# Kernel tuning notes

Measured on AMD Instinct MI355X. Metric: run time of the kernel, lower is better.

## Reference

```python
import jax, jax.numpy as jnp
import numpy as np

LN_EPS = 1e-5
B, T, D, H, NB, HH = 256, 128, 512, 1024, 64, 8


def _layernorm(x, g, b):
    m = x.mean(-1, keepdims=True)
    v = ((x - m) ** 2).mean(-1, keepdims=True)
    return (x - m) / jnp.sqrt(v + LN_EPS) * g + b


def setup_inputs() -> dict:
    key = jax.random.key(0)
    ks = jax.random.split(key, 10)
    init = lambda k, shape, fan: jax.random.normal(k, shape, jnp.float32) * np.float32(1.0 / np.sqrt(fan))
    return {
        "context_features": jax.random.normal(ks[0], (B, T, D), jnp.float32),
        "beam_history": jax.random.randint(ks[1], (B, HH), 0, NB),
        "beam_embed": init(ks[2], (NB, D), D),
        "W_in": init(ks[3], (H, 2 * D), 2 * D), "b_in": jnp.zeros((H,), jnp.float32),
        "W_init": init(ks[4], (H, 2 * D), 2 * D), "b_init": jnp.zeros((H,), jnp.float32),
        "W_ih": init(ks[5], (3 * H, H), H), "b_ih": jnp.zeros((3 * H,), jnp.float32),
        "W_hh": init(ks[6], (3 * H, H), H), "b_hh": jnp.zeros((3 * H,), jnp.float32),
        "ln_g": jnp.ones((H,), jnp.float32), "ln_b": jnp.zeros((H,), jnp.float32),
        "W_o1": init(ks[7], (H, H + D), H + D), "b_o1": jnp.zeros((H,), jnp.float32),
        "W_o2": init(ks[8], (NB, H), H), "b_o2": jnp.zeros((NB,), jnp.float32),
    }


def reference(context_features, beam_history, beam_embed, W_in, b_in, W_init, b_init,
              W_ih, b_ih, W_hh, b_hh, ln_g, ln_b, W_o1, b_o1, W_o2, b_o2):
    # --- init: history embedding mean + global context mean -> initial GRU state ---
    prev0 = beam_history[:, -1]                      # (B,)
    hist_emb = beam_embed[beam_history].mean(axis=1)  # (B, D)
    ctx_global = context_features.mean(axis=1)        # (B, D)
    h0 = jnp.tanh(jnp.concatenate([ctx_global, hist_emb], axis=-1) @ W_init.T + b_init)  # (B, H)

    def step(carry, ctx_t):
        h, prev = carry
        prev_emb = beam_embed[prev]                                            # (B, D)
        x = jax.nn.relu(jnp.concatenate([ctx_t, prev_emb], -1) @ W_in.T + b_in)  # (B, H)
        # PyTorch GRUCell: gate order r, z, n
        gx = x @ W_ih.T + b_ih
        gh = h @ W_hh.T + b_hh
        xr, xz, xn = jnp.split(gx, 3, axis=-1)
        hr, hz, hn = jnp.split(gh, 3, axis=-1)
        r = jax.nn.sigmoid(xr + hr)
        z = jax.nn.sigmoid(xz + hz)
        n = jnp.tanh(xn + r * hn)
        h_new = (1.0 - z) * n + z * h
        h_norm = _layernorm(h_new, ln_g, ln_b)
        o = jax.nn.relu(jnp.concatenate([h_norm, ctx_t], -1) @ W_o1.T + b_o1)
        logits_t = o @ W_o2.T + b_o2                                            # (B, NB)
        pred_next = jnp.argmax(logits_t, axis=-1)
        return (h_new, pred_next), logits_t

    ctx_tbd = jnp.swapaxes(context_features, 0, 1)  # (T, B, D)
    (_, _), logits = jax.lax.scan(step, (h0, prev0), ctx_tbd)
    return jnp.swapaxes(logits, 0, 1)  # (B, T, NB) == ar_logits
```

## Files before the change

kernel.cpp:

```cpp
#include <hip/hip_runtime.h>
#include <hip/hip_bf16.h>


#define TS 68
#define LDPA 40
constexpr int SZ = 262144;
constexpr int TT = 128;
constexpr int LDA_CTX = 65536;

typedef __attribute__((ext_vector_type(8))) short short8_t;
typedef __attribute__((ext_vector_type(4))) float f32x4;


__device__ __forceinline__ unsigned short f2bf_rne(float v) {
    unsigned u = __float_as_uint(v);
    unsigned r = u + 0x7fffu + ((u >> 16) & 1u);
    return (unsigned short)(r >> 16);
}
__device__ __forceinline__ float bfbits2f(unsigned short h) {
    return __uint_as_float(((unsigned)h) << 16);
}
__device__ __forceinline__ void split2(float v, unsigned short& h, unsigned short& l) {
    h = f2bf_rne(v);
    l = f2bf_rne(v - bfbits2f(h));
}


__device__ __forceinline__ void mfma_core7(
    const unsigned short* __restrict__ Ah, const unsigned short* __restrict__ Al,
    int lda, int b0,
    const unsigned short* __restrict__ Bh, const unsigned short* __restrict__ Bl,
    int ldb, int n0, int k0base, int nIter,
    unsigned short* sm, f32x4 acc[2][4])
{
    const int tid = threadIdx.x, lane = tid & 63, wid = tid >> 6;
    const int wr = wid >> 1, wc = wid & 1;
    const int l15 = lane & 15, kg = (lane >> 4) * 8;
    const int arow = tid >> 2, acol = (tid & 3) * 8;
    const int brow = tid >> 1, bcol = (tid & 1) * 16;

    const int AOFF = 2560, BHOFF = 5120, BLOFF = 10240, BUF = 15360;

    const unsigned short* gAh = Ah + (size_t)(b0 + arow) * lda + k0base + acol;
    const unsigned short* gAl = Al + (size_t)(b0 + arow) * lda + k0base + acol;
    const unsigned short* gBh = Bh + (size_t)(n0 + brow) * ldb + k0base + bcol;
    const unsigned short* gBl = Bl + (size_t)(n0 + brow) * ldb + k0base + bcol;

    {
        short8_t a_h = *(const short8_t*)gAh;
        short8_t a_l = *(const short8_t*)gAl;
        short8_t bh0 = *(const short8_t*)gBh;
        short8_t bh1 = *(const short8_t*)(gBh + 8);
        short8_t bl0 = *(const short8_t*)gBl;
        short8_t bl1 = *(const short8_t*)(gBl + 8);
        *(short8_t*)&sm[arow * LDPA + acol]              = a_h;
        *(short8_t*)&sm[AOFF + arow * LDPA + acol]       = a_l;
        *(short8_t*)&sm[BHOFF + brow * LDPA + bcol]      = bh0;
        *(short8_t*)&sm[BHOFF + brow * LDPA + bcol + 8]  = bh1;
        *(short8_t*)&sm[BLOFF + brow * LDPA + bcol]      = bl0;
        *(short8_t*)&sm[BLOFF + brow * LDPA + bcol + 8]  = bl1;
    }
    __syncthreads();

    int cur = 0;
    const int aro = (wr * 32 + l15) * LDPA + kg;
    for (int i = 0; i < nIter; ++i) {
        short8_t a_h, a_l, bh0, bh1, bl0, bl1;
        if (i + 1 < nIter) {
            const int ko = (i + 1) * 32;
            a_h = *(const short8_t*)(gAh + ko);
            a_l = *(const short8_t*)(gAl + ko);
            bh0 = *(const short8_t*)(gBh + ko);
            bh1 = *(const short8_t*)(gBh + ko + 8);
            bl0 = *(const short8_t*)(gBl + ko);
            bl1 = *(const short8_t*)(gBl + ko + 8);
        }
        const unsigned short* S = sm + cur * BUF;
        short8_t afh[2], afl[2];
#pragma unroll
        for (int mi = 0; mi < 2; ++mi) {
            afh[mi] = *(const short8_t*)&S[aro + mi * 16 * LDPA];
            afl[mi] = *(const short8_t*)&S[AOFF + aro + mi * 16 * LDPA];
        }
#pragma unroll
        for (int ni = 0; ni < 4; ++ni) {
            const int bro = (wc * 64 + ni * 16 + l15) * LDPA + kg;
            short8_t b_h = *(const short8_t*)&S[BHOFF + bro];
            short8_t b_l = *(const short8_t*)&S[BLOFF + bro];
#pragma unroll
            for (int mi = 0; mi < 2; ++mi) {
                acc[mi][ni] = __builtin_amdgcn_mfma_f32_16x16x32_bf16(afh[mi], b_h, acc[mi][ni], 0, 0, 0);
                acc[mi][ni] = __builtin_amdgcn_mfma_f32_16x16x32_bf16(afh[mi], b_l, acc[mi][ni], 0, 0, 0);
                acc[mi][ni] = __builtin_amdgcn_mfma_f32_16x16x32_bf16(afl[mi], b_h, acc[mi][ni], 0, 0, 0);
            }
        }
        if (i + 1 < nIter) {
            unsigned short* N_ = sm + (cur ^ 1) * BUF;
            *(short8_t*)&N_[arow * LDPA + acol]             = a_h;
            *(short8_t*)&N_[AOFF + arow * LDPA + acol]      = a_l;
            *(short8_t*)&N_[BHOFF + brow * LDPA + bcol]     = bh0;
            *(short8_t*)&N_[BHOFF + brow * LDPA + bcol + 8] = bh1;
            *(short8_t*)&N_[BLOFF + brow * LDPA + bcol]     = bl0;
            *(short8_t*)&N_[BLOFF + brow * LDPA + bcol + 8] = bl1;
        }
        __syncthreads();
        cur ^= 1;
    }
}


__device__ __forceinline__ void gemm_tile64(
    const float* __restrict__ A, int lda, int Mlim, int b0,
    const float* __restrict__ W, int ldw, int n0, int K,
    float* At, float* Wt, float acc[4][4])
{
    const int tid = threadIdx.x;
    const int tx = tid & 15, ty = tid >> 4;
    const int r = tid >> 2, c0 = (tid & 3) << 2;
    for (int k0 = 0; k0 < K; k0 += 16) {
        float4 av = make_float4(0.f, 0.f, 0.f, 0.f);
        if (b0 + r < Mlim)
            av = *(const float4*)(A + (size_t)(b0 + r) * lda + k0 + c0);
        float4 wv = *(const float4*)(W + (size_t)(n0 + r) * ldw + k0 + c0);
        __syncthreads();
        At[(c0+0)*TS + r] = av.x; At[(c0+1)*TS + r] = av.y;
        At[(c0+2)*TS + r] = av.z; At[(c0+3)*TS + r] = av.w;
        Wt[(c0+0)*TS + r] = wv.x; Wt[(c0+1)*TS + r] = wv.y;
        Wt[(c0+2)*TS + r] = wv.z; Wt[(c0+3)*TS + r] = wv.w;
        __syncthreads();
#pragma unroll
        for (int kk = 0; kk < 16; ++kk) {
            float4 a = *(const float4*)(At + kk*TS + ty*4);
            float4 w = *(const float4*)(Wt + kk*TS + tx*4);
            acc[0][0] += a.x*w.x; acc[0][1] += a.x*w.y; acc[0][2] += a.x*w.z; acc[0][3] += a.x*w.w;
            acc[1][0] += a.y*w.x; acc[1][1] += a.y*w.y; acc[1][2] += a.y*w.z; acc[1][3] += a.y*w.w;
            acc[2][0] += a.z*w.x; acc[2][1] += a.z*w.y; acc[2][2] += a.z*w.z; acc[2][3] += a.z*w.w;
            acc[3][0] += a.w*w.x; acc[3][1] += a.w*w.y; acc[3][2] += a.w*w.z; acc[3][3] += a.w*w.w;
        }
    }
}


__global__ void pre0_kernel(const float* __restrict__ ctx, const int* __restrict__ bh,
                            const float* __restrict__ be, float* __restrict__ A0,
                            int* __restrict__ prev)
{
    int b = blockIdx.x, tid = threadIdx.x;
    float s = 0.f;
    for (int t = 0; t < TT; ++t) s += ctx[(size_t)b * LDA_CTX + t * 512 + tid];
    A0[b * 1024 + tid] = s * (1.f / 128.f);
    float s2 = 0.f;
    for (int i = 0; i < 8; ++i) s2 += be[bh[b * 8 + i] * 512 + tid];
    A0[b * 1024 + 512 + tid] = s2 * 0.125f;
    if (tid == 0) prev[b] = bh[b * 8 + 7];
}

__global__ void copy_gb_kernel(const float* g, const float* bb, float* gb)
{
    int idx = blockIdx.x * 256 + threadIdx.x;
    if (idx < 1024) gb[idx] = g[idx];
    else            gb[idx] = bb[idx - 1024];
}

__global__ void wo2t_kernel(const float* __restrict__ W_o2, float* __restrict__ Wo2t)
{
    int idx = blockIdx.x * 256 + threadIdx.x;
    int k = idx >> 6, n = idx & 63;
    Wo2t[idx] = W_o2[n * 1024 + k];
}

__global__ void wsplit_kernel(const float* __restrict__ src, int src_ld, int col0,
                              int N, int K, const float* __restrict__ scale,
                              unsigned short* __restrict__ hi,
                              unsigned short* __restrict__ lo)
{
    int idx = blockIdx.x * 256 + threadIdx.x;
    if (idx >= N * K) return;
    int n = idx / K, k = idx - n * K;
    float v = src[(size_t)n * src_ld + col0 + k];
    if (scale) v *= scale[k];
    unsigned short h, l;
    split2(v, h, l);
    hi[idx] = h; lo[idx] = l;
}

__global__ void gemm64_kernel(const float* __restrict__ A, int lda, int M,
                              const float* __restrict__ W, int ldw, int K,
                              const float* __restrict__ bias,
                              float* __restrict__ C, int ldc, int act)
{
    __shared__ __align__(16) float At[16 * TS];
    __shared__ __align__(16) float Wt[16 * TS];
    float acc[4][4] = {};
    int b0 = blockIdx.x * 64, n0 = blockIdx.y * 64;
    gemm_tile64(A, lda, M, b0, W, ldw, n0, K, At, Wt, acc);
    int tx = threadIdx.x & 15, ty = threadIdx.x >> 4;
#pragma unroll
    for (int i = 0; i < 4; ++i) {
        int b = b0 + ty * 4 + i;
        if (b >= M) continue;
#pragma unroll
        for (int j = 0; j < 4; ++j) {
            int n = n0 + tx * 4 + j;
            float v = acc[i][j] + (bias ? bias[n] : 0.f);
            if (act == 1) v = tanhf(v);
            C[(size_t)b * ldc + n] = v;
        }
    }
}

__global__ void xbuild0s_kernel(const float* __restrict__ cin0, const float* __restrict__ bpart,
                                const int* __restrict__ prev,
                                unsigned short* __restrict__ xh, unsigned short* __restrict__ xl)
{
    int b = blockIdx.x, tid = threadIdx.x;
    int pb = prev[b];
#pragma unroll
    for (int jj = 0; jj < 4; ++jj) {
        int j = jj * 256 + tid;
        float v = fmaxf(cin0[(size_t)b * 1024 + j] + bpart[(size_t)pb * 1024 + j], 0.f);
        unsigned short h, l;
        split2(v, h, l);
        xh[(size_t)b * 1024 + j] = h;
        xl[(size_t)b * 1024 + j] = l;
    }
}

__global__ void xbuild0_kernel(const float* __restrict__ cin0, const float* __restrict__ bpart,
                               const int* __restrict__ prev, float* __restrict__ x)
{
    int b = blockIdx.x, tid = threadIdx.x;
    int pb = prev[b];
#pragma unroll
    for (int jj = 0; jj < 4; ++jj) {
        int j = jj * 256 + tid;
        x[(size_t)b * 1024 + j] = fmaxf(cin0[(size_t)b * 1024 + j] + bpart[(size_t)pb * 1024 + j], 0.f);
    }
}


__global__ __launch_bounds__(256) void gates7_kernel(
    const unsigned short* __restrict__ xh, const unsigned short* __restrict__ xl,
    const unsigned short* __restrict__ hh, const unsigned short* __restrict__ hl,
    const unsigned short* __restrict__ ctxh, const unsigned short* __restrict__ ctxl,
    const unsigned short* __restrict__ wih_hi, const unsigned short* __restrict__ wih_lo,
    const unsigned short* __restrict__ whh_hi, const unsigned short* __restrict__ whh_lo,
    const unsigned short* __restrict__ wcin_hi, const unsigned short* __restrict__ wcin_lo,
    const unsigned short* __restrict__ wo1c_hi, const unsigned short* __restrict__ wo1c_lo,
    const float* __restrict__ b_in, const float* __restrict__ b_o1,
    float* __restrict__ g6, float* __restrict__ cin, float* __restrict__ octx,
    int t)
{
    const int bid = blockIdx.x;
    const int z = bid & 7;
    const int tile = bid >> 3;
    const int tm = tile & 3, tn = tile >> 2;
    if (z == 6 && t + 1 >= TT) return;
    const int b0 = tm * 64, n0 = tn * 128;

    const unsigned short *Ah, *Al, *Bh, *Bl;
    int lda, ldb, nIter;
    const float* bias = nullptr;
    float* C;
    if (z < 6) {
        int g = z % 3, s = z / 3;
        Ah = s ? hh : xh; Al = s ? hl : xl; lda = 1024;
        Bh = (s ? whh_hi : wih_hi) + (size_t)g * 1048576;
        Bl = (s ? whh_lo : wih_lo) + (size_t)g * 1048576;
        ldb = 1024; nIter = 32;
        C = g6 + (size_t)z * SZ;
    } else if (z == 6) {
        int s = (t + 1) & 1;
        Ah = ctxh + (size_t)s * 131072; Al = ctxl + (size_t)s * 131072;
        lda = 512; ldb = 512; nIter = 16;
        Bh = wcin_hi; Bl = wcin_lo; bias = b_in; C = cin;
    } else {
        int s = t & 1;
        Ah = ctxh + (size_t)s * 131072; Al = ctxl + (size_t)s * 131072;
        lda = 512; ldb = 512; nIter = 16;
        Bh = wo1c_hi; Bl = wo1c_lo; bias = b_o1; C = octx;
    }

    __shared__ __align__(16) unsigned short sm[2 * 15360];
    f32x4 acc[2][4] = {};
    mfma_core7(Ah, Al, lda, b0, Bh, Bl, ldb, n0, 0, nIter, sm, acc);

    const int lane = threadIdx.x & 63, wid = threadIdx.x >> 6;
    const int wr = wid >> 1, wc = wid & 1;
    const int l15 = lane & 15, g4 = (lane >> 4) * 4;
#pragma unroll
    for (int mi = 0; mi < 2; ++mi) {
#pragma unroll
        for (int ni = 0; ni < 4; ++ni) {
            int col = n0 + wc * 64 + ni * 16 + l15;
            float bv = bias ? bias[col] : 0.f;
#pragma unroll
            for (int r = 0; r < 4; ++r) {
                int row = b0 + wr * 32 + mi * 16 + g4 + r;
                C[(size_t)row * 1024 + col] = acc[mi][ni][r] + bv;
            }
        }
    }
}

__global__ __launch_bounds__(256) void kb7_kernel(
    const unsigned short* __restrict__ hh, const unsigned short* __restrict__ hl,
    const unsigned short* __restrict__ wo1k_hi, const unsigned short* __restrict__ wo1k_lo,
    float* __restrict__ g6)
{
    const int bid = blockIdx.x;
    const int tm = bid >> 5, tn = (bid >> 2) & 7, p = bid & 3;
    const int b0 = tm * 64, n0 = tn * 128, k0 = p * 256;

    __shared__ __align__(16) unsigned short sm[2 * 15360];
    f32x4 acc[2][4] = {};
    mfma_core7(hh, hl, 1024, b0, wo1k_hi, wo1k_lo, 1024, n0, k0, 8, sm, acc);

    float* C = g6 + (size_t)p * SZ;
    const int lane = threadIdx.x & 63, wid = threadIdx.x >> 6;
    const int wr = wid >> 1, wc = wid & 1;
    const int l15 = lane & 15, g4 = (lane >> 4) * 4;
#pragma unroll
    for (int mi = 0; mi < 2; ++mi) {
#pragma unroll
        for (int ni = 0; ni < 4; ++ni) {
            int col = n0 + wc * 64 + ni * 16 + l15;
#pragma unroll
            for (int r = 0; r < 4; ++r) {
                int row = b0 + wr * 32 + mi * 16 + g4 + r;
                C[(size_t)row * 1024 + col] = acc[mi][ni][r];
            }
        }
    }
}

__global__ void gru_ln6_kernel(const float* __restrict__ g6,
                               const float* __restrict__ b_ih, const float* __restrict__ b_hh,
                               float* __restrict__ h,
                               unsigned short* __restrict__ hh, unsigned short* __restrict__ hl,
                               float* __restrict__ mbuf, float* __restrict__ isbuf)
{
    __shared__ float ls[4], lq[4];
    int b = blockIdx.x, tid = threadIdx.x;
    float s = 0.f, q = 0.f;
#pragma unroll
    for (int jj = 0; jj < 4; ++jj) {
        int j = jj * 256 + tid;
        size_t base = (size_t)b * 1024 + j;
        float xr = g6[0 * (size_t)SZ + base] + b_ih[j];
        float xz = g6[1 * (size_t)SZ + base] + b_ih[1024 + j];
        float xn = g6[2 * (size_t)SZ + base] + b_ih[2048 + j];
        float hr = g6[3 * (size_t)SZ + base] + b_hh[j];
        float hz = g6[4 * (size_t)SZ + base] + b_hh[1024 + j];
        float hn = g6[5 * (size_t)SZ + base] + b_hh[2048 + j];
        float r = 1.f / (1.f + expf(-(xr + hr)));
        float z = 1.f / (1.f + expf(-(xz + hz)));
        float nn = tanhf(xn + r * hn);
        float ho = h[base];
        float hv = (1.f - z) * nn + z * ho;
        h[base] = hv;
        unsigned short a, c;
        split2(hv, a, c); hh[base] = a; hl[base] = c;
        s += hv; q += hv * hv;
    }
    for (int off = 32; off; off >>= 1) {
        s += __shfl_down(s, off);
        q += __shfl_down(q, off);
    }
    int lane = tid & 63, w = tid >> 6;
    if (lane == 0) { ls[w] = s; lq[w] = q; }
    __syncthreads();
    if (tid == 0) {
        float S = ls[0] + ls[1] + ls[2] + ls[3];
        float Q = lq[0] + lq[1] + lq[2] + lq[3];
        float m = S * (1.f / 1024.f);
        mbuf[b] = m;
        isbuf[b] = rsqrtf(Q * (1.f / 1024.f) - m * m + 1e-5f);
    }
}

__global__ void kc7_kernel(const float* __restrict__ g6,
                           const float* __restrict__ Wo2t, const float* __restrict__ b_o2,
                           const float* __restrict__ uv, const float* __restrict__ octx,
                           const float* __restrict__ mbuf, const float* __restrict__ isbuf,
                           const float* __restrict__ cin, const float* __restrict__ bpart,
                           const float* __restrict__ ctx,
                           unsigned short* __restrict__ xh, unsigned short* __restrict__ xl,
                           unsigned short* __restrict__ ctxh, unsigned short* __restrict__ ctxl,
                           int* __restrict__ prev, float* __restrict__ out, int t)
{
    __shared__ __align__(16) float os[4][1024];
    __shared__ float red[4][4][64];
    __shared__ int sidx[4];
    const int b0 = blockIdx.x * 4, tid = threadIdx.x;

#pragma unroll
    for (int i = 0; i < 4; ++i) {
        int f = tid + i * 256;
        int r = f >> 8, c4 = (f & 255) << 2;
        size_t base = (size_t)(b0 + r) * 1024 + c4;
        float4 p0 = *(const float4*)(g6 + base);
        float4 p1 = *(const float4*)(g6 + (size_t)SZ + base);
        float4 p2 = *(const float4*)(g6 + 2 * (size_t)SZ + base);
        float4 p3 = *(const float4*)(g6 + 3 * (size_t)SZ + base);
        float4 oc = *(const float4*)(octx + base);
        float4 u4 = *(const float4*)(uv + c4);
        float4 v4 = *(const float4*)(uv + 1024 + c4);
        float m = mbuf[b0 + r], is = isbuf[b0 + r];
        float4 o4;
        o4.x = fmaxf((p0.x + p1.x + p2.x + p3.x - m * u4.x) * is + v4.x + oc.x, 0.f);
        o4.y = fmaxf((p0.y + p1.y + p2.y + p3.y - m * u4.y) * is + v4.y + oc.y, 0.f);
        o4.z = fmaxf((p0.z + p1.z + p2.z + p3.z - m * u4.z) * is + v4.z + oc.z, 0.f);
        o4.w = fmaxf((p0.w + p1.w + p2.w + p3.w - m * u4.w) * is + v4.w + oc.w, 0.f);
        *(float4*)&os[r][c4] = o4;
    }
    __syncthreads();

    {
        int n = tid & 63, seg = tid >> 6;
        float p0 = 0.f, p1 = 0.f, p2 = 0.f, p3 = 0.f;
        int k0 = seg * 256;
        for (int k = k0; k < k0 + 256; ++k) {
            float w = Wo2t[(size_t)k * 64 + n];
            p0 += os[0][k] * w; p1 += os[1][k] * w;
            p2 += os[2][k] * w; p3 += os[3][k] * w;
        }
        red[0][seg][n] = p0; red[1][seg][n] = p1;
        red[2][seg][n] = p2; red[3][seg][n] = p3;
    }
    __syncthreads();

    {
        int r = tid >> 6, n = tid & 63;
        float lg = red[r][0][n] + red[r][1][n] + red[r][2][n] + red[r][3][n] + b_o2[n];
        out[(size_t)(b0 + r) * (TT * 64) + t * 64 + n] = lg;
        float v = lg; int idx = n;
        for (int off = 32; off; off >>= 1) {
            float ov = __shfl_xor(v, off);
            int oi = __shfl_xor(idx, off);
            if (ov > v || (ov == v && oi < idx)) { v = ov; idx = oi; }
        }
        if (n == 0) { prev[b0 + r] = idx; sidx[r] = idx; }
    }
    __syncthreads();

    if (t + 1 < TT) {
#pragma unroll
        for (int i = 0; i < 16; ++i) {
            int idx = tid + i * 256;
            int r = idx >> 10, j = idx & 1023;
            float v = fmaxf(cin[(size_t)(b0 + r) * 1024 + j] +
                            bpart[(size_t)sidx[r] * 1024 + j], 0.f);
            unsigned short h, l;
            split2(v, h, l);
            xh[(size_t)(b0 + r) * 1024 + j] = h;
            xl[(size_t)(b0 + r) * 1024 + j] = l;
        }
    }
    if (t + 2 < TT) {
        int slot = t & 1;
#pragma unroll
        for (int i = 0; i < 8; ++i) {
            int idx = tid + i * 256;
            int r = idx >> 9, j = idx & 511;
            float v = ctx[(size_t)(b0 + r) * LDA_CTX + (t + 2) * 512 + j];
            unsigned short h, l;
            split2(v, h, l);
            ctxh[(size_t)slot * 131072 + (size_t)(b0 + r) * 512 + j] = h;
            ctxl[(size_t)slot * 131072 + (size_t)(b0 + r) * 512 + j] = l;
        }
    }
}


__global__ void step_gemms_kernel(
    const float* __restrict__ x, const float* __restrict__ hBase,
    const float* __restrict__ ctx,
    const float* __restrict__ Wih, const float* __restrict__ Whh,
    const float* __restrict__ Win, const float* __restrict__ Wo1,
    const float* __restrict__ b_in, const float* __restrict__ b_o1,
    float* __restrict__ g6, float* __restrict__ cinBase, float* __restrict__ octx,
    int t)
{
    __shared__ __align__(16) float At[16 * TS];
    __shared__ __align__(16) float Wt[16 * TS];
    float acc[4][4] = {};
    const int z = blockIdx.z, b0 = blockIdx.x * 64, n0 = blockIdx.y * 64;
    const float *A, *W, *bias = nullptr;
    float* C;
    int lda, ldw, K;
    if (z < 6) {
        int g = z % 3, s = z / 3;
        A = s ? (hBase + (size_t)(t & 1) * SZ) : x;
        lda = 1024;
        W = (s ? Whh : Wih) + (size_t)(g * 1024) * 1024;
        ldw = 1024; K = 1024;
        C = g6 + (size_t)z * SZ;
    } else if (z == 6) {
        if (t + 1 >= TT) return;
        A = ctx + (size_t)(t + 1) * 512; lda = LDA_CTX;
        W = Win; ldw = 1024; K = 512; bias = b_in;
        C = cinBase + (size_t)((t + 1) & 1) * SZ;
    } else {
        A = ctx + (size_t)t * 512; lda = LDA_CTX;
        W = Wo1 + 1024; ldw = 1536; K = 512; bias = b_o1;
        C = octx;
    }
    gemm_tile64(A, lda, 256, b0, W, ldw, n0, K, At, Wt, acc);
    int tx = threadIdx.x & 15, ty = threadIdx.x >> 4;
#pragma unroll
    for (int i = 0; i < 4; ++i) {
        int b = b0 + ty * 4 + i;
#pragma unroll
        for (int j = 0; j < 4; ++j) {
            int n = n0 + tx * 4 + j;
            float v = acc[i][j];
            if (bias) v += bias[n];
            C[(size_t)b * 1024 + n] = v;
        }
    }
}

__global__ void kb_kernel(const float* __restrict__ hg, const float* __restrict__ Wo1,
                          const float* __restrict__ uv, const float* __restrict__ octx,
                          const float* __restrict__ mbuf, const float* __restrict__ isbuf,
                          float* __restrict__ o)
{
    __shared__ __align__(16) float At[16 * TS];
    __shared__ __align__(16) float Wt[16 * TS];
    float acc[2][4] = {};
    const int b0 = blockIdx.x * 32, n0 = blockIdx.y * 64;
    const int tid = threadIdx.x, tx = tid & 15, ty = tid >> 4;
    const int r = tid >> 2, c0 = (tid & 3) << 2;
    for (int k0 = 0; k0 < 1024; k0 += 16) {
        float4 av = make_float4(0.f, 0.f, 0.f, 0.f);
        if (r < 32) av = *(const float4*)(hg + (size_t)(b0 + r) * 1024 + k0 + c0);
        float4 wv = *(const float4*)(Wo1 + (size_t)(n0 + r) * 1536 + k0 + c0);
        __syncthreads();
        At[(c0+0)*TS + r] = av.x; At[(c0+1)*TS + r] = av.y;
        At[(c0+2)*TS + r] = av.z; At[(c0+3)*TS + r] = av.w;
        Wt[(c0+0)*TS + r] = wv.x; Wt[(c0+1)*TS + r] = wv.y;
        Wt[(c0+2)*TS + r] = wv.z; Wt[(c0+3)*TS + r] = wv.w;
        __syncthreads();
#pragma unroll
        for (int kk = 0; kk < 16; ++kk) {
            float2 a = *(const float2*)(At + kk*TS + ty*2);
            float4 w = *(const float4*)(Wt + kk*TS + tx*4);
            acc[0][0] += a.x*w.x; acc[0][1] += a.x*w.y; acc[0][2] += a.x*w.z; acc[0][3] += a.x*w.w;
            acc[1][0] += a.y*w.x; acc[1][1] += a.y*w.y; acc[1][2] += a.y*w.z; acc[1][3] += a.y*w.w;
        }
    }
#pragma unroll
    for (int i = 0; i < 2; ++i) {
        int b = b0 + ty * 2 + i;
        float m = mbuf[b], is = isbuf[b];
#pragma unroll
        for (int j = 0; j < 4; ++j) {
            int n = n0 + tx * 4 + j;
            float v = (acc[i][j] - m * uv[n]) * is + uv[1024 + n] + octx[(size_t)b * 1024 + n];
            o[(size_t)b * 1024 + n] = fmaxf(v, 0.f);
        }
    }
}

__global__ void gru_ln_kernel(const float* __restrict__ g6,
                              const float* __restrict__ b_ih, const float* __restrict__ b_hh,
                              float* __restrict__ hBase, const float* __restrict__ ln_g,
                              float* __restrict__ hg, float* __restrict__ mbuf,
                              float* __restrict__ isbuf, int t)
{
    __shared__ float rs[256], rq[256];
    int b = blockIdx.x, tid = threadIdx.x;
    const float* hc = hBase + (size_t)(t & 1) * SZ + (size_t)b * 1024;
    float* hnx = hBase + (size_t)((t + 1) & 1) * SZ + (size_t)b * 1024;
    float s = 0.f, q = 0.f;
#pragma unroll
    for (int jj = 0; jj < 4; ++jj) {
        int j = jj * 256 + tid;
        size_t base = (size_t)b * 1024 + j;
        float xr = g6[0 * (size_t)SZ + base] + b_ih[j];
        float xz = g6[1 * (size_t)SZ + base] + b_ih[1024 + j];
        float xn = g6[2 * (size_t)SZ + base] + b_ih[2048 + j];
        float hr = g6[3 * (size_t)SZ + base] + b_hh[j];
        float hz = g6[4 * (size_t)SZ + base] + b_hh[1024 + j];
        float hn = g6[5 * (size_t)SZ + base] + b_hh[2048 + j];
        float r = 1.f / (1.f + expf(-(xr + hr)));
        float z = 1.f / (1.f + expf(-(xz + hz)));
        float nn = tanhf(xn + r * hn);
        float ho = hc[j];
        float hv = (1.f - z) * nn + z * ho;
        hnx[j] = hv;
        hg[base] = hv * ln_g[j];
        s += hv; q += hv * hv;
    }
    rs[tid] = s; rq[tid] = q;
    __syncthreads();
    for (int st = 128; st; st >>= 1) {
        if (tid < st) { rs[tid] += rs[tid + st]; rq[tid] += rq[tid + st]; }
        __syncthreads();
    }
    if (tid == 0) {
        float m = rs[0] * (1.f / 1024.f);
        float var = rq[0] * (1.f / 1024.f) - m * m;
        mbuf[b] = m;
        isbuf[b] = rsqrtf(var + 1e-5f);
    }
}

__global__ void kc_kernel(const float* __restrict__ o, const float* __restrict__ Wo2t,
                          const float* __restrict__ b_o2, const float* __restrict__ cinBase,
                          const float* __restrict__ bpart, float* __restrict__ x,
                          int* __restrict__ prev, float* __restrict__ out, int t)
{
    __shared__ __align__(16) float os[1024];
    __shared__ float red[4][64];
    __shared__ int sidx;
    int b = blockIdx.x, tid = threadIdx.x;
    const float* orow = o + (size_t)b * 1024;
    *(float4*)&os[tid * 4] = *(const float4*)&orow[tid * 4];
    __syncthreads();
    int n = tid & 63, seg = tid >> 6;
    float p = 0.f;
    int k0 = seg * 256;
#pragma unroll 8
    for (int k = 0; k < 256; ++k) p += os[k0 + k] * Wo2t[(size_t)(k0 + k) * 64 + n];
    red[seg][n] = p;
    __syncthreads();
    if (tid < 64) {
        float lg = red[0][tid] + red[1][tid] + red[2][tid] + red[3][tid] + b_o2[tid];
        out[((size_t)b * TT + t) * 64 + tid] = lg;
        float v = lg; int idx = tid;
        for (int off = 32; off; off >>= 1) {
            float ov = __shfl_xor(v, off);
            int oi = __shfl_xor(idx, off);
            if (ov > v || (ov == v && oi < idx)) { v = ov; idx = oi; }
        }
        if (tid == 0) { prev[b] = idx; sidx = idx; }
    }
    __syncthreads();
    if (t + 1 < TT) {
        int pb = sidx;
        const float* cn = cinBase + (size_t)((t + 1) & 1) * SZ + (size_t)b * 1024;
        const float* bp = bpart + (size_t)pb * 1024;
#pragma unroll
        for (int jj = 0; jj < 4; ++jj) {
            int j = jj * 256 + tid;
            x[(size_t)b * 1024 + j] = fmaxf(cn[j] + bp[j], 0.f);
        }
    }
}


extern "C" void kernel_launch(void* const* d_in, const int* in_sizes, int n_in,
                              void* d_out, int out_size, void* d_ws, size_t ws_size,
                              hipStream_t stream)
{
    const float* ctx    = (const float*)d_in[0];
    const int*   bh     = (const int*)d_in[1];
    const float* be     = (const float*)d_in[2];
    const float* W_in   = (const float*)d_in[3];
    const float* b_in   = (const float*)d_in[4];
    const float* W_init = (const float*)d_in[5];
    const float* b_init = (const float*)d_in[6];
    const float* W_ih   = (const float*)d_in[7];
    const float* b_ih   = (const float*)d_in[8];
    const float* W_hh   = (const float*)d_in[9];
    const float* b_hh   = (const float*)d_in[10];
    const float* ln_g   = (const float*)d_in[11];
    const float* ln_b   = (const float*)d_in[12];
    const float* W_o1   = (const float*)d_in[13];
    const float* b_o1   = (const float*)d_in[14];
    const float* W_o2   = (const float*)d_in[15];
    const float* b_o2   = (const float*)d_in[16];
    float* out = (float*)d_out;
    float* ws  = (float*)d_ws;

    const bool mfma_path = (ws_size >= 49830000ull);

    if (mfma_path) {
        float* hbuf  = ws;
        float* cin   = ws + 262144;
        float* octx  = ws + 524288;
        float* g6    = ws + 786432;
        float* A0    = g6;
        float* bpart = ws + 2359296;
        float* uvv   = ws + 2424832;
        float* gb    = ws + 2426880;
        float* Wo2t  = ws + 2428928;
        float* mbuf  = ws + 2494464;
        float* isbuf = ws + 2494720;
        int*   prev  = (int*)(ws + 2494976);
        unsigned short* bf = (unsigned short*)(ws + 2495232);
        unsigned short* wih_hi  = bf;
        unsigned short* wih_lo  = bf + 3145728;
        unsigned short* whh_hi  = bf + 6291456;
        unsigned short* whh_lo  = bf + 9437184;
        unsigned short* wo1k_hi = bf + 12582912;
        unsigned short* wo1k_lo = bf + 13631488;
        unsigned short* wo1c_hi = bf + 14680064;
        unsigned short* wo1c_lo = bf + 15204352;
        unsigned short* wcin_hi = bf + 15728640;
        unsigned short* wcin_lo = bf + 16252928;
        unsigned short* xh   = bf + 16777216;
        unsigned short* xl   = bf + 17039360;
        unsigned short* hh   = bf + 17301504;
        unsigned short* hl   = bf + 17563648;
        unsigned short* ctxh = bf + 17825792;
        unsigned short* ctxl = bf + 18087936;

        pre0_kernel<<<256, 512, 0, stream>>>(ctx, bh, be, A0, prev);
        copy_gb_kernel<<<8, 256, 0, stream>>>(ln_g, ln_b, gb);
        wo2t_kernel<<<256, 256, 0, stream>>>(W_o2, Wo2t);
        gemm64_kernel<<<dim3(4, 16), 256, 0, stream>>>(A0, 1024, 256, W_init, 1024, 1024,
                                                       b_init, hbuf, 1024, 1);
        gemm64_kernel<<<dim3(1, 16), 256, 0, stream>>>(be, 512, 64, W_in + 512, 1024, 512,
                                                       nullptr, bpart, 1024, 0);
        gemm64_kernel<<<dim3(1, 16), 256, 0, stream>>>(gb, 1024, 2, W_o1, 1536, 1024,
                                                       nullptr, uvv, 1024, 0);
        gemm64_kernel<<<dim3(4, 16), 256, 0, stream>>>(ctx, LDA_CTX, 256, W_in, 1024, 512,
                                                       b_in, cin, 1024, 0);
        xbuild0s_kernel<<<256, 256, 0, stream>>>(cin, bpart, prev, xh, xl);
        wsplit_kernel<<<12288, 256, 0, stream>>>(W_ih, 1024, 0, 3072, 1024, nullptr, wih_hi, wih_lo);
        wsplit_kernel<<<12288, 256, 0, stream>>>(W_hh, 1024, 0, 3072, 1024, nullptr, whh_hi, whh_lo);
        wsplit_kernel<<<4096, 256, 0, stream>>>(W_o1, 1536, 0, 1024, 1024, ln_g, wo1k_hi, wo1k_lo);
        wsplit_kernel<<<2048, 256, 0, stream>>>(W_o1, 1536, 1024, 1024, 512, nullptr, wo1c_hi, wo1c_lo);
        wsplit_kernel<<<2048, 256, 0, stream>>>(W_in, 1024, 0, 1024, 512, nullptr, wcin_hi, wcin_lo);
        wsplit_kernel<<<1024, 256, 0, stream>>>(hbuf, 1024, 0, 256, 1024, nullptr, hh, hl);
        wsplit_kernel<<<512, 256, 0, stream>>>(ctx, LDA_CTX, 0, 256, 512, nullptr, ctxh, ctxl);
        wsplit_kernel<<<512, 256, 0, stream>>>(ctx, LDA_CTX, 512, 256, 512, nullptr,
                                               ctxh + 131072, ctxl + 131072);

        for (int t = 0; t < TT; ++t) {
            gates7_kernel<<<256, 256, 0, stream>>>(
                xh, xl, hh, hl, ctxh, ctxl,
                wih_hi, wih_lo, whh_hi, whh_lo, wcin_hi, wcin_lo, wo1c_hi, wo1c_lo,
                b_in, b_o1, g6, cin, octx, t);
            gru_ln6_kernel<<<256, 256, 0, stream>>>(g6, b_ih, b_hh, hbuf,
                                                    hh, hl, mbuf, isbuf);
            kb7_kernel<<<128, 256, 0, stream>>>(hh, hl, wo1k_hi, wo1k_lo, g6);
            kc7_kernel<<<64, 256, 0, stream>>>(g6, Wo2t, b_o2, uvv, octx, mbuf, isbuf,
                                               cin, bpart, ctx, xh, xl, ctxh, ctxl,
                                               prev, out, t);
        }
    } else {
        float* A0    = ws;
        float* hbuf  = ws + 262144;
        float* hg    = ws + 786432;
        float* x     = ws + 1048576;
        float* cin   = ws + 1310720;
        float* octx  = ws + 1835008;
        float* g6    = ws + 2097152;
        float* obuf  = ws + 3670016;
        float* bpart = ws + 3932160;
        float* uvv   = ws + 3997696;
        float* gb    = ws + 3999744;
        float* Wo2t  = ws + 4001792;
        float* mbuf  = ws + 4067328;
        float* isbuf = ws + 4067584;
        int*   prev  = (int*)(ws + 4067840);

        pre0_kernel<<<256, 512, 0, stream>>>(ctx, bh, be, A0, prev);
        copy_gb_kernel<<<8, 256, 0, stream>>>(ln_g, ln_b, gb);
        wo2t_kernel<<<256, 256, 0, stream>>>(W_o2, Wo2t);
        gemm64_kernel<<<dim3(4, 16), 256, 0, stream>>>(A0, 1024, 256, W_init, 1024, 1024,
                                                       b_init, hbuf, 1024, 1);
        gemm64_kernel<<<dim3(1, 16), 256, 0, stream>>>(be, 512, 64, W_in + 512, 1024, 512,
                                                       nullptr, bpart, 1024, 0);
        gemm64_kernel<<<dim3(1, 16), 256, 0, stream>>>(gb, 1024, 2, W_o1, 1536, 1024,
                                                       nullptr, uvv, 1024, 0);
        gemm64_kernel<<<dim3(4, 16), 256, 0, stream>>>(ctx, LDA_CTX, 256, W_in, 1024, 512,
                                                       b_in, cin, 1024, 0);
        xbuild0_kernel<<<256, 256, 0, stream>>>(cin, bpart, prev, x);

        for (int t = 0; t < TT; ++t) {
            step_gemms_kernel<<<dim3(4, 16, 8), 256, 0, stream>>>(
                x, hbuf, ctx, W_ih, W_hh, W_in, W_o1, b_in, b_o1, g6, cin, octx, t);
            gru_ln_kernel<<<256, 256, 0, stream>>>(g6, b_ih, b_hh, hbuf, ln_g, hg,
                                                   mbuf, isbuf, t);
            kb_kernel<<<dim3(8, 16), 256, 0, stream>>>(hg, W_o1, uvv, octx, mbuf, isbuf, obuf);
            kc_kernel<<<256, 256, 0, stream>>>(obuf, Wo2t, b_o2, cin, bpart, x, prev, out, t);
        }
    }
}
```

Before: 7.913 ms.

## Fuse GRU+LayerNorm stats into output GEMM kernel and split fp32 activations on the fly

The separate GRU/LayerNorm kernel is folded into the kb kernel. Each block recomputes the GRU update for its 64x256 slice, writes h to a double-buffered fp32 array, and emits partial LN sums that kc combines. Activations (x, h, ctx) are now read as fp32 in the MFMA core and split into bf16 hi/lo while being staged into shared memory. This removes the pre-split hi/lo buffers, the ctx prefetch split, and one launch per timestep. In exchange, each block does extra split arithmetic in the inner loop, and the GRU elementwise work is repeated across the 8 column-tile blocks that share rows.

```diff
diff --git a/kernel.cpp b/kernel.cpp
--- a/kernel.cpp
+++ b/kernel.cpp
@@ -24,11 +24,22 @@
     h = f2bf_rne(v);
     l = f2bf_rne(v - bfbits2f(h));
 }
-
-
-__device__ __forceinline__ void mfma_core7(
-    const unsigned short* __restrict__ Ah, const unsigned short* __restrict__ Al,
-    int lda, int b0,
+__device__ __forceinline__ void splitA8(const float4& v0, const float4& v1,
+                                        short8_t& hi, short8_t& lo) {
+    unsigned short h[8], l[8];
+    split2(v0.x, h[0], l[0]); split2(v0.y, h[1], l[1]);
+    split2(v0.z, h[2], l[2]); split2(v0.w, h[3], l[3]);
+    split2(v1.x, h[4], l[4]); split2(v1.y, h[5], l[5]);
+    split2(v1.z, h[6], l[6]); split2(v1.w, h[7], l[7]);
+    hi = short8_t{(short)h[0],(short)h[1],(short)h[2],(short)h[3],
+                  (short)h[4],(short)h[5],(short)h[6],(short)h[7]};
+    lo = short8_t{(short)l[0],(short)l[1],(short)l[2],(short)l[3],
+                  (short)l[4],(short)l[5],(short)l[6],(short)l[7]};
+}
+
+
+__device__ __forceinline__ void mfma_core9(
+    const float* __restrict__ A, int lda, int b0,
     const unsigned short* __restrict__ Bh, const unsigned short* __restrict__ Bl,
     int ldb, int n0, int k0base, int nIter,
     unsigned short* sm, f32x4 acc[2][4])
@@ -41,20 +52,21 @@
 
     const int AOFF = 2560, BHOFF = 5120, BLOFF = 10240, BUF = 15360;
 
-    const unsigned short* gAh = Ah + (size_t)(b0 + arow) * lda + k0base + acol;
-    const unsigned short* gAl = Al + (size_t)(b0 + arow) * lda + k0base + acol;
+    const float* gA = A + (size_t)(b0 + arow) * lda + k0base + acol;
     const unsigned short* gBh = Bh + (size_t)(n0 + brow) * ldb + k0base + bcol;
     const unsigned short* gBl = Bl + (size_t)(n0 + brow) * ldb + k0base + bcol;
 
     {
-        short8_t a_h = *(const short8_t*)gAh;
-        short8_t a_l = *(const short8_t*)gAl;
+        float4 a0 = *(const float4*)gA;
+        float4 a1 = *(const float4*)(gA + 4);
+        short8_t ah, al;
+        splitA8(a0, a1, ah, al);
         short8_t bh0 = *(const short8_t*)gBh;
         short8_t bh1 = *(const short8_t*)(gBh + 8);
         short8_t bl0 = *(const short8_t*)gBl;
         short8_t bl1 = *(const short8_t*)(gBl + 8);
-        *(short8_t*)&sm[arow * LDPA + acol]              = a_h;
-        *(short8_t*)&sm[AOFF + arow * LDPA + acol]       = a_l;
+        *(short8_t*)&sm[arow * LDPA + acol]              = ah;
+        *(short8_t*)&sm[AOFF + arow * LDPA + acol]       = al;
         *(short8_t*)&sm[BHOFF + brow * LDPA + bcol]      = bh0;
         *(short8_t*)&sm[BHOFF + brow * LDPA + bcol + 8]  = bh1;
         *(short8_t*)&sm[BLOFF + brow * LDPA + bcol]      = bl0;
@@ -65,11 +77,12 @@
     int cur = 0;
     const int aro = (wr * 32 + l15) * LDPA + kg;
     for (int i = 0; i < nIter; ++i) {
-        short8_t a_h, a_l, bh0, bh1, bl0, bl1;
+        float4 a0, a1;
+        short8_t bh0, bh1, bl0, bl1;
         if (i + 1 < nIter) {
             const int ko = (i + 1) * 32;
-            a_h = *(const short8_t*)(gAh + ko);
-            a_l = *(const short8_t*)(gAl + ko);
+            a0 = *(const float4*)(gA + ko);
+            a1 = *(const float4*)(gA + ko + 4);
             bh0 = *(const short8_t*)(gBh + ko);
             bh1 = *(const short8_t*)(gBh + ko + 8);
             bl0 = *(const short8_t*)(gBl + ko);
@@ -95,9 +108,11 @@
             }
         }
         if (i + 1 < nIter) {
+            short8_t ah, al;
+            splitA8(a0, a1, ah, al);
             unsigned short* N_ = sm + (cur ^ 1) * BUF;
-            *(short8_t*)&N_[arow * LDPA + acol]             = a_h;
-            *(short8_t*)&N_[AOFF + arow * LDPA + acol]      = a_l;
+            *(short8_t*)&N_[arow * LDPA + acol]             = ah;
+            *(short8_t*)&N_[AOFF + arow * LDPA + acol]      = al;
             *(short8_t*)&N_[BHOFF + brow * LDPA + bcol]     = bh0;
             *(short8_t*)&N_[BHOFF + brow * LDPA + bcol + 8] = bh1;
             *(short8_t*)&N_[BLOFF + brow * LDPA + bcol]     = bl0;
@@ -155,18 +170,22 @@
     if (tid == 0) prev[b] = bh[b * 8 + 7];
 }
 
-__global__ void copy_gb_kernel(const float* g, const float* bb, float* gb)
-{
-    int idx = blockIdx.x * 256 + threadIdx.x;
-    if (idx < 1024) gb[idx] = g[idx];
-    else            gb[idx] = bb[idx - 1024];
-}
-
 __global__ void wo2t_kernel(const float* __restrict__ W_o2, float* __restrict__ Wo2t)
 {
     int idx = blockIdx.x * 256 + threadIdx.x;
     int k = idx >> 6, n = idx & 63;
     Wo2t[idx] = W_o2[n * 1024 + k];
+}
+
+__global__ void uv_kernel(const float* __restrict__ ln_g, const float* __restrict__ ln_b,
+                          const float* __restrict__ W_o1, float* __restrict__ uvv)
+{
+    int idx = blockIdx.x * 256 + threadIdx.x;
+    int which = idx >> 10, j = idx & 1023;
+    const float* vec = which ? ln_b : ln_g;
+    float s = 0.f;
+    for (int k = 0; k < 1024; ++k) s += vec[k] * W_o1[(size_t)j * 1536 + k];
+    uvv[which * 1024 + j] = s;
 }
 
 __global__ void wsplit_kernel(const float* __restrict__ src, int src_ld, int col0,
@@ -209,23 +228,6 @@
     }
 }
 
-__global__ void xbuild0s_kernel(const float* __restrict__ cin0, const float* __restrict__ bpart,
-                                const int* __restrict__ prev,
-                                unsigned short* __restrict__ xh, unsigned short* __restrict__ xl)
-{
-    int b = blockIdx.x, tid = threadIdx.x;
-    int pb = prev[b];
-#pragma unroll
-    for (int jj = 0; jj < 4; ++jj) {
-        int j = jj * 256 + tid;
-        float v = fmaxf(cin0[(size_t)b * 1024 + j] + bpart[(size_t)pb * 1024 + j], 0.f);
-        unsigned short h, l;
-        split2(v, h, l);
-        xh[(size_t)b * 1024 + j] = h;
-        xl[(size_t)b * 1024 + j] = l;
-    }
-}
-
 __global__ void xbuild0_kernel(const float* __restrict__ cin0, const float* __restrict__ bpart,
                                const int* __restrict__ prev, float* __restrict__ x)
 {
@@ -239,10 +241,9 @@
 }
 
 
-__global__ __launch_bounds__(256) void gates7_kernel(
-    const unsigned short* __restrict__ xh, const unsigned short* __restrict__ xl,
-    const unsigned short* __restrict__ hh, const unsigned short* __restrict__ hl,
-    const unsigned short* __restrict__ ctxh, const unsigned short* __restrict__ ctxl,
+__global__ __launch_bounds__(256) void gates9_kernel(
+    const float* __restrict__ xf, const float* __restrict__ hcur,
+    const float* __restrict__ ctx,
     const unsigned short* __restrict__ wih_hi, const unsigned short* __restrict__ wih_lo,
     const unsigned short* __restrict__ whh_hi, const unsigned short* __restrict__ whh_lo,
     const unsigned short* __restrict__ wcin_hi, const unsigned short* __restrict__ wcin_lo,
@@ -258,32 +259,31 @@
     if (z == 6 && t + 1 >= TT) return;
     const int b0 = tm * 64, n0 = tn * 128;
 
-    const unsigned short *Ah, *Al, *Bh, *Bl;
+    const float* A;
+    const unsigned short *Bh, *Bl;
     int lda, ldb, nIter;
     const float* bias = nullptr;
     float* C;
     if (z < 6) {
         int g = z % 3, s = z / 3;
-        Ah = s ? hh : xh; Al = s ? hl : xl; lda = 1024;
+        A = s ? hcur : xf; lda = 1024;
         Bh = (s ? whh_hi : wih_hi) + (size_t)g * 1048576;
         Bl = (s ? whh_lo : wih_lo) + (size_t)g * 1048576;
         ldb = 1024; nIter = 32;
         C = g6 + (size_t)z * SZ;
     } else if (z == 6) {
-        int s = (t + 1) & 1;
-        Ah = ctxh + (size_t)s * 131072; Al = ctxl + (size_t)s * 131072;
-        lda = 512; ldb = 512; nIter = 16;
+        A = ctx + (size_t)(t + 1) * 512; lda = LDA_CTX;
+        ldb = 512; nIter = 16;
         Bh = wcin_hi; Bl = wcin_lo; bias = b_in; C = cin;
     } else {
-        int s = t & 1;
-        Ah = ctxh + (size_t)s * 131072; Al = ctxl + (size_t)s * 131072;
-        lda = 512; ldb = 512; nIter = 16;
+        A = ctx + (size_t)t * 512; lda = LDA_CTX;
+        ldb = 512; nIter = 16;
         Bh = wo1c_hi; Bl = wo1c_lo; bias = b_o1; C = octx;
     }
 
     __shared__ __align__(16) unsigned short sm[2 * 15360];
     f32x4 acc[2][4] = {};
-    mfma_core7(Ah, Al, lda, b0, Bh, Bl, ldb, n0, 0, nIter, sm, acc);
+    mfma_core9(A, lda, b0, Bh, Bl, ldb, n0, 0, nIter, sm, acc);
 
     const int lane = threadIdx.x & 63, wid = threadIdx.x >> 6;
     const int wr = wid >> 1, wc = wid & 1;
@@ -303,21 +303,83 @@
     }
 }
 
-__global__ __launch_bounds__(256) void kb7_kernel(
-    const unsigned short* __restrict__ hh, const unsigned short* __restrict__ hl,
+__global__ __launch_bounds__(256) void kb9_kernel(
+    const float* __restrict__ g6,
+    const float* __restrict__ b_ih, const float* __restrict__ b_hh,
+    const float* __restrict__ hOld, float* __restrict__ hNew,
     const unsigned short* __restrict__ wo1k_hi, const unsigned short* __restrict__ wo1k_lo,
-    float* __restrict__ g6)
+    float* __restrict__ part, float* __restrict__ spq)
 {
     const int bid = blockIdx.x;
-    const int tm = bid >> 5, tn = (bid >> 2) & 7, p = bid & 3;
+    const int g = bid & 15, tn = bid >> 4;
+    const int tm = g >> 2, p = g & 3;
     const int b0 = tm * 64, n0 = tn * 128, k0 = p * 256;
+    const int tid = threadIdx.x;
+
+    {
+        const int r = tid >> 2, q = tid & 3;
+        const int row = b0 + r;
+        float s = 0.f, qs = 0.f;
+        for (int j = 0; j < 16; ++j) {
+            int c = k0 + j * 16 + q * 4;
+            size_t base = (size_t)row * 1024 + c;
+            float4 xr = *(const float4*)(g6 + base);
+            float4 xz = *(const float4*)(g6 + (size_t)SZ + base);
+            float4 xn = *(const float4*)(g6 + 2 * (size_t)SZ + base);
+            float4 hr = *(const float4*)(g6 + 3 * (size_t)SZ + base);
+            float4 hz = *(const float4*)(g6 + 4 * (size_t)SZ + base);
+            float4 hn = *(const float4*)(g6 + 5 * (size_t)SZ + base);
+            float4 ho = *(const float4*)(hOld + base);
+            float4 bi0 = *(const float4*)(b_ih + c);
+            float4 bi1 = *(const float4*)(b_ih + 1024 + c);
+            float4 bi2 = *(const float4*)(b_ih + 2048 + c);
+            float4 bh0 = *(const float4*)(b_hh + c);
+            float4 bh1 = *(const float4*)(b_hh + 1024 + c);
+            float4 bh2 = *(const float4*)(b_hh + 2048 + c);
+            float4 hv;
+            {
+                float rr = 1.f / (1.f + expf(-((xr.x + bi0.x) + (hr.x + bh0.x))));
+                float zz = 1.f / (1.f + expf(-((xz.x + bi1.x) + (hz.x + bh1.x))));
+                float nn = tanhf((xn.x + bi2.x) + rr * (hn.x + bh2.x));
+                hv.x = (1.f - zz) * nn + zz * ho.x;
+            }
+            {
+                float rr = 1.f / (1.f + expf(-((xr.y + bi0.y) + (hr.y + bh0.y))));
+                float zz = 1.f / (1.f + expf(-((xz.y + bi1.y) + (hz.y + bh1.y))));
+                float nn = tanhf((xn.y + bi2.y) + rr * (hn.y + bh2.y));
+                hv.y = (1.f - zz) * nn + zz * ho.y;
+            }
+            {
+                float rr = 1.f / (1.f + expf(-((xr.z + bi0.z) + (hr.z + bh0.z))));
+                float zz = 1.f / (1.f + expf(-((xz.z + bi1.z) + (hz.z + bh1.z))));
+                float nn = tanhf((xn.z + bi2.z) + rr * (hn.z + bh2.z));
+                hv.z = (1.f - zz) * nn + zz * ho.z;
+            }
+            {
+                float rr = 1.f / (1.f + expf(-((xr.w + bi0.w) + (hr.w + bh0.w))));
+                float zz = 1.f / (1.f + expf(-((xz.w + bi1.w) + (hz.w + bh1.w))));
+                float nn = tanhf((xn.w + bi2.w) + rr * (hn.w + bh2.w));
+                hv.w = (1.f - zz) * nn + zz * ho.w;
+            }
+            *(float4*)(hNew + base) = hv;
+            s += hv.x + hv.y + hv.z + hv.w;
+            qs += hv.x * hv.x + hv.y * hv.y + hv.z * hv.z + hv.w * hv.w;
+        }
+        s  += __shfl_xor(s, 1);  s  += __shfl_xor(s, 2);
+        qs += __shfl_xor(qs, 1); qs += __shfl_xor(qs, 2);
+        if (q == 0) {
+            spq[(p * 256 + row) * 2]     = s;
+            spq[(p * 256 + row) * 2 + 1] = qs;
+        }
+    }
+    __syncthreads();
 
     __shared__ __align__(16) unsigned short sm[2 * 15360];
     f32x4 acc[2][4] = {};
-    mfma_core7(hh, hl, 1024, b0, wo1k_hi, wo1k_lo, 1024, n0, k0, 8, sm, acc);
-
-    float* C = g6 + (size_t)p * SZ;
-    const int lane = threadIdx.x & 63, wid = threadIdx.x >> 6;
+    mfma_core9(hNew, 1024, b0, wo1k_hi, wo1k_lo, 1024, n0, k0, 8, sm, acc);
+
+    float* C = part + (size_t)p * SZ;
+    const int lane = tid & 63, wid = tid >> 6;
     const int wr = wid >> 1, wc = wid & 1;
     const int l15 = lane & 15, g4 = (lane >> 4) * 4;
 #pragma unroll
@@ -334,79 +396,44 @@
     }
 }
 
-__global__ void gru_ln6_kernel(const float* __restrict__ g6,
-                               const float* __restrict__ b_ih, const float* __restrict__ b_hh,
-                               float* __restrict__ h,
-                               unsigned short* __restrict__ hh, unsigned short* __restrict__ hl,
-                               float* __restrict__ mbuf, float* __restrict__ isbuf)
-{
-    __shared__ float ls[4], lq[4];
-    int b = blockIdx.x, tid = threadIdx.x;
-    float s = 0.f, q = 0.f;
-#pragma unroll
-    for (int jj = 0; jj < 4; ++jj) {
-        int j = jj * 256 + tid;
-        size_t base = (size_t)b * 1024 + j;
-        float xr = g6[0 * (size_t)SZ + base] + b_ih[j];
-        float xz = g6[1 * (size_t)SZ + base] + b_ih[1024 + j];
-        float xn = g6[2 * (size_t)SZ + base] + b_ih[2048 + j];
-        float hr = g6[3 * (size_t)SZ + base] + b_hh[j];
-        float hz = g6[4 * (size_t)SZ + base] + b_hh[1024 + j];
-        float hn = g6[5 * (size_t)SZ + base] + b_hh[2048 + j];
-        float r = 1.f / (1.f + expf(-(xr + hr)));
-        float z = 1.f / (1.f + expf(-(xz + hz)));
-        float nn = tanhf(xn + r * hn);
-        float ho = h[base];
-        float hv = (1.f - z) * nn + z * ho;
-        h[base] = hv;
-        unsigned short a, c;
-        split2(hv, a, c); hh[base] = a; hl[base] = c;
-        s += hv; q += hv * hv;
-    }
-    for (int off = 32; off; off >>= 1) {
-        s += __shfl_down(s, off);
-        q += __shfl_down(q, off);
-    }
-    int lane = tid & 63, w = tid >> 6;
-    if (lane == 0) { ls[w] = s; lq[w] = q; }
-    __syncthreads();
-    if (tid == 0) {
-        float S = ls[0] + ls[1] + ls[2] + ls[3];
-        float Q = lq[0] + lq[1] + lq[2] + lq[3];
-        float m = S * (1.f / 1024.f);
-        mbuf[b] = m;
-        isbuf[b] = rsqrtf(Q * (1.f / 1024.f) - m * m + 1e-5f);
-    }
-}
-
-__global__ void kc7_kernel(const float* __restrict__ g6,
+__global__ void kc9_kernel(const float* __restrict__ part, const float* __restrict__ spq,
                            const float* __restrict__ Wo2t, const float* __restrict__ b_o2,
                            const float* __restrict__ uv, const float* __restrict__ octx,
-                           const float* __restrict__ mbuf, const float* __restrict__ isbuf,
                            const float* __restrict__ cin, const float* __restrict__ bpart,
-                           const float* __restrict__ ctx,
-                           unsigned short* __restrict__ xh, unsigned short* __restrict__ xl,
-                           unsigned short* __restrict__ ctxh, unsigned short* __restrict__ ctxl,
+                           float* __restrict__ xf,
                            int* __restrict__ prev, float* __restrict__ out, int t)
 {
     __shared__ __align__(16) float os[4][1024];
     __shared__ float red[4][4][64];
+    __shared__ float sm_m[4], sm_is[4];
     __shared__ int sidx[4];
     const int b0 = blockIdx.x * 4, tid = threadIdx.x;
+
+    if (tid < 4) {
+        int row = b0 + tid;
+        float s = spq[(0 * 256 + row) * 2] + spq[(1 * 256 + row) * 2]
+                + spq[(2 * 256 + row) * 2] + spq[(3 * 256 + row) * 2];
+        float qq = spq[(0 * 256 + row) * 2 + 1] + spq[(1 * 256 + row) * 2 + 1]
+                 + spq[(2 * 256 + row) * 2 + 1] + spq[(3 * 256 + row) * 2 + 1];
+        float m = s * (1.f / 1024.f);
+        sm_m[tid] = m;
+        sm_is[tid] = rsqrtf(qq * (1.f / 1024.f) - m * m + 1e-5f);
+    }
+    __syncthreads();
 
 #pragma unroll
     for (int i = 0; i < 4; ++i) {
         int f = tid + i * 256;
         int r = f >> 8, c4 = (f & 255) << 2;
         size_t base = (size_t)(b0 + r) * 1024 + c4;
-        float4 p0 = *(const float4*)(g6 + base);
-        float4 p1 = *(const float4*)(g6 + (size_t)SZ + base);
-        float4 p2 = *(const float4*)(g6 + 2 * (size_t)SZ + base);
-        float4 p3 = *(const float4*)(g6 + 3 * (size_t)SZ + base);
+        float4 p0 = *(const float4*)(part + base);
+        float4 p1 = *(const float4*)(part + (size_t)SZ + base);
+        float4 p2 = *(const float4*)(part + 2 * (size_t)SZ + base);
+        float4 p3 = *(const float4*)(part + 3 * (size_t)SZ + base);
         float4 oc = *(const float4*)(octx + base);
         float4 u4 = *(const float4*)(uv + c4);
         float4 v4 = *(const float4*)(uv + 1024 + c4);
-        float m = mbuf[b0 + r], is = isbuf[b0 + r];
+        float m = sm_m[r], is = sm_is[r];
         float4 o4;
         o4.x = fmaxf((p0.x + p1.x + p2.x + p3.x - m * u4.x) * is + v4.x + oc.x, 0.f);
         o4.y = fmaxf((p0.y + p1.y + p2.y + p3.y - m * u4.y) * is + v4.y + oc.y, 0.f);
@@ -449,25 +476,9 @@
         for (int i = 0; i < 16; ++i) {
             int idx = tid + i * 256;
             int r = idx >> 10, j = idx & 1023;
-            float v = fmaxf(cin[(size_t)(b0 + r) * 1024 + j] +
-                            bpart[(size_t)sidx[r] * 1024 + j], 0.f);
-            unsigned short h, l;
-            split2(v, h, l);
-            xh[(size_t)(b0 + r) * 1024 + j] = h;
-            xl[(size_t)(b0 + r) * 1024 + j] = l;
-        }
-    }
-    if (t + 2 < TT) {
-        int slot = t & 1;
-#pragma unroll
-        for (int i = 0; i < 8; ++i) {
-            int idx = tid + i * 256;
-            int r = idx >> 9, j = idx & 511;
-            float v = ctx[(size_t)(b0 + r) * LDA_CTX + (t + 2) * 512 + j];
-            unsigned short h, l;
-            split2(v, h, l);
-            ctxh[(size_t)slot * 131072 + (size_t)(b0 + r) * 512 + j] = h;
-            ctxl[(size_t)slot * 131072 + (size_t)(b0 + r) * 512 + j] = l;
+            xf[(size_t)(b0 + r) * 1024 + j] =
+                fmaxf(cin[(size_t)(b0 + r) * 1024 + j] +
+                      bpart[(size_t)sidx[r] * 1024 + j], 0.f);
         }
     }
 }
@@ -650,6 +661,13 @@
     }
 }
 
+__global__ void copy_gb_kernel(const float* g, const float* bb, float* gb)
+{
+    int idx = blockIdx.x * 256 + threadIdx.x;
+    if (idx < 1024) gb[idx] = g[idx];
+    else            gb[idx] = bb[idx - 1024];
+}
+
 
 extern "C" void kernel_launch(void* const* d_in, const int* in_sizes, int n_in,
                               void* d_out, int out_size, void* d_ws, size_t ws_size,
@@ -679,18 +697,18 @@
 
     if (mfma_path) {
         float* hbuf  = ws;
-        float* cin   = ws + 262144;
-        float* octx  = ws + 524288;
-        float* g6    = ws + 786432;
+        float* cin   = ws + 524288;
+        float* octx  = ws + 786432;
+        float* g6    = ws + 1048576;
         float* A0    = g6;
-        float* bpart = ws + 2359296;
-        float* uvv   = ws + 2424832;
-        float* gb    = ws + 2426880;
-        float* Wo2t  = ws + 2428928;
-        float* mbuf  = ws + 2494464;
-        float* isbuf = ws + 2494720;
-        int*   prev  = (int*)(ws + 2494976);
-        unsigned short* bf = (unsigned short*)(ws + 2495232);
+        float* part  = ws + 2621440;
+        float* xf    = ws + 3670016;
+        float* bpart = ws + 3932160;
+        float* uvv   = ws + 3997696;
+        float* Wo2t  = ws + 3999744;
+        float* spq   = ws + 4065280;
+        int*   prev  = (int*)(ws + 4067328);
+        unsigned short* bf = (unsigned short*)(ws + 4067840);
         unsigned short* wih_hi  = bf;
         unsigned short* wih_lo  = bf + 3145728;
         unsigned short* whh_hi  = bf + 6291456;
@@ -701,46 +719,34 @@
         unsigned short* wo1c_lo = bf + 15204352;
         unsigned short* wcin_hi = bf + 15728640;
         unsigned short* wcin_lo = bf + 16252928;
-        unsigned short* xh   = bf + 16777216;
-        unsigned short* xl   = bf + 17039360;
-        unsigned short* hh   = bf + 17301504;
-        unsigned short* hl   = bf + 17563648;
-        unsigned short* ctxh = bf + 17825792;
-        unsigned short* ctxl = bf + 18087936;
 
         pre0_kernel<<<256, 512, 0, stream>>>(ctx, bh, be, A0, prev);
-        copy_gb_kernel<<<8, 256, 0, stream>>>(ln_g, ln_b, gb);
         wo2t_kernel<<<256, 256, 0, stream>>>(W_o2, Wo2t);
+        uv_kernel<<<8, 256, 0, stream>>>(ln_g, ln_b, W_o1, uvv);
         gemm64_kernel<<<dim3(4, 16), 256, 0, stream>>>(A0, 1024, 256, W_init, 1024, 1024,
                                                        b_init, hbuf, 1024, 1);
         gemm64_kernel<<<dim3(1, 16), 256, 0, stream>>>(be, 512, 64, W_in + 512, 1024, 512,
                                                        nullptr, bpart, 1024, 0);
-        gemm64_kernel<<<dim3(1, 16), 256, 0, stream>>>(gb, 1024, 2, W_o1, 1536, 1024,
-                                                       nullptr, uvv, 1024, 0);
         gemm64_kernel<<<dim3(4, 16), 256, 0, stream>>>(ctx, LDA_CTX, 256, W_in, 1024, 512,
                                                        b_in, cin, 1024, 0);
-        xbuild0s_kernel<<<256, 256, 0, stream>>>(cin, bpart, prev, xh, xl);
+        xbuild0_kernel<<<256, 256, 0, stream>>>(cin, bpart, prev, xf);
         wsplit_kernel<<<12288, 256, 0, stream>>>(W_ih, 1024, 0, 3072, 1024, nullptr, wih_hi, wih_lo);
         wsplit_kernel<<<12288, 256, 0, stream>>>(W_hh, 1024, 0, 3072, 1024, nullptr, whh_hi, whh_lo);
         wsplit_kernel<<<4096, 256, 0, stream>>>(W_o1, 1536, 0, 1024, 1024, ln_g, wo1k_hi, wo1k_lo);
         wsplit_kernel<<<2048, 256, 0, stream>>>(W_o1, 1536, 1024, 1024, 512, nullptr, wo1c_hi, wo1c_lo);
         wsplit_kernel<<<2048, 256, 0, stream>>>(W_in, 1024, 0, 1024, 512, nullptr, wcin_hi, wcin_lo);
-        wsplit_kernel<<<1024, 256, 0, stream>>>(hbuf, 1024, 0, 256, 1024, nullptr, hh, hl);
-        wsplit_kernel<<<512, 256, 0, stream>>>(ctx, LDA_CTX, 0, 256, 512, nullptr, ctxh, ctxl);
-        wsplit_kernel<<<512, 256, 0, stream>>>(ctx, LDA_CTX, 512, 256, 512, nullptr,
-                                               ctxh + 131072, ctxl + 131072);
 
         for (int t = 0; t < TT; ++t) {
-            gates7_kernel<<<256, 256, 0, stream>>>(
-                xh, xl, hh, hl, ctxh, ctxl,
+            const float* hcur = hbuf + (size_t)(t & 1) * SZ;
+            float* hnew = hbuf + (size_t)((t + 1) & 1) * SZ;
+            gates9_kernel<<<256, 256, 0, stream>>>(
+                xf, hcur, ctx,
                 wih_hi, wih_lo, whh_hi, whh_lo, wcin_hi, wcin_lo, wo1c_hi, wo1c_lo,
                 b_in, b_o1, g6, cin, octx, t);
-            gru_ln6_kernel<<<256, 256, 0, stream>>>(g6, b_ih, b_hh, hbuf,
-                                                    hh, hl, mbuf, isbuf);
-            kb7_kernel<<<128, 256, 0, stream>>>(hh, hl, wo1k_hi, wo1k_lo, g6);
-            kc7_kernel<<<64, 256, 0, stream>>>(g6, Wo2t, b_o2, uvv, octx, mbuf, isbuf,
-                                               cin, bpart, ctx, xh, xl, ctxh, ctxl,
-                                               prev, out, t);
+            kb9_kernel<<<128, 256, 0, stream>>>(g6, b_ih, b_hh, hcur, hnew,
+                                                wo1k_hi, wo1k_lo, part, spq);
+            kc9_kernel<<<64, 256, 0, stream>>>(part, spq, Wo2t, b_o2, uvv, octx,
+                                               cin, bpart, xf, prev, out, t);
         }
     } else {
         float* A0    = ws;
```

Result: slower. 10.35 ms (+30.7%).
